# Kernel tuning notes

Hardware: AMD Instinct MI355X
Metric: run time of the kernel (lower is better)

The kernel has to match this reference:

```python
import jax, jax.numpy as jnp
import numpy as np

N = 38332          # poi_len - 1 nodes
POI_LEN = 38333
GF = 64            # graph_features
POI_DIM = 128
C = 128            # gcn_channel
L = 4              # gcn_layers
OUT = 128          # graph_out_dim
E = N * 16         # edges (avg degree 16)
IN_DIM = POI_DIM * GF // 2 + GF // 2  # 4128


def leaky(x, s):
    return jnp.where(x >= 0, x, s * x)


def _gcn(x, W, b, src, dst):
    # PyG GCNConv: lin -> symmetric deg^{-1/2} norm over self-loop graph -> scatter-sum + bias
    h = x @ W
    deg = jax.ops.segment_sum(jnp.ones(src.shape[0], h.dtype), dst, num_segments=N)
    dinv = jnp.where(deg > 0, jax.lax.rsqrt(deg), 0.0)
    norm = dinv[src] * dinv[dst]
    return jax.ops.segment_sum(h[src] * norm[:, None], dst, num_segments=N) + b


def _gat(x, W, a_src, a_dst, b, src, dst):
    # PyG GATConv (heads=1): per-edge LeakyReLU(0.2) logits, softmax over incoming edges
    h = x @ W
    als = h @ a_src            # [N]
    ald = h @ a_dst            # [N]
    e = leaky(als[src] + ald[dst], 0.2)   # [E+N]
    m = jax.ops.segment_max(e, dst, num_segments=N)
    ex = jnp.exp(e - m[dst])
    s = jax.ops.segment_sum(ex, dst, num_segments=N)
    alpha = ex / s[dst]
    return jax.ops.segment_sum(h[src] * alpha[:, None], dst, num_segments=N) + b


def _gnorm(x, w, b, ms, eps=1e-5):
    # PyG GraphNorm over the single graph (node axis)
    mean = x.mean(axis=0)
    out = x - ms * mean
    var = (out * out).mean(axis=0)
    return w * out * jax.lax.rsqrt(var + eps) + b


def setup_inputs() -> dict:
    key = jax.random.key(0)
    ks = jax.random.split(key, 20)
    d = {}
    d["poi"] = jax.random.randint(ks[0], (N, GF // 2), 0, POI_LEN, dtype=jnp.int32)
    d["distance"] = jax.random.uniform(ks[1], (N, GF // 2), dtype=jnp.float32)
    d["edge_index"] = jax.random.randint(ks[2], (2, E), 0, N, dtype=jnp.int32)
    d["emb_table"] = jax.random.normal(ks[3], (POI_LEN, POI_DIM), dtype=jnp.float32) * 0.05
    d["W_in"] = jax.random.normal(ks[4], (IN_DIM, C), dtype=jnp.float32) * 0.02
    d["b_in"] = jnp.zeros((C,), jnp.float32)
    d["gcn_W"] = jax.random.normal(ks[5], (L, C, C), dtype=jnp.float32) * 0.05
    d["gcn_b"] = jnp.zeros((L, C), jnp.float32)
    d["norm_w"] = jnp.ones((L, C), jnp.float32)
    d["norm_b"] = jnp.zeros((L, C), jnp.float32)
    d["norm_ms"] = jnp.ones((L, C), jnp.float32)
    d["gat_W"] = jax.random.normal(ks[6], (L, C, C), dtype=jnp.float32) * 0.05
    d["gat_asrc"] = jax.random.normal(ks[7], (L, C), dtype=jnp.float32) * 0.05
    d["gat_adst"] = jax.random.normal(ks[8], (L, C), dtype=jnp.float32) * 0.05
    d["gat_b"] = jnp.zeros((L, C), jnp.float32)
    d["W_out"] = jax.random.normal(ks[9], (C, 1), dtype=jnp.float32) * 0.05
    d["b_out"] = jnp.zeros((1,), jnp.float32)
    d["fc1_W"] = jax.random.normal(ks[10], (N, 128), dtype=jnp.float32) * 0.01
    d["fc1_b"] = jnp.zeros((128,), jnp.float32)
    d["fc2_W"] = jax.random.normal(ks[11], (128, OUT), dtype=jnp.float32) * 0.05
    d["fc2_b"] = jnp.zeros((OUT,), jnp.float32)
    return d


def reference(poi, distance, edge_index, emb_table, W_in, b_in, gcn_W, gcn_b,
              norm_w, norm_b, norm_ms, gat_W, gat_asrc, gat_adst, gat_b,
              W_out, b_out, fc1_W, fc1_b, fc2_W, fc2_b):
    loops = jnp.arange(N, dtype=edge_index.dtype)
    src = jnp.concatenate([edge_index[0], loops])   # self loops (PyG default)
    dst = jnp.concatenate([edge_index[1], loops])
    # feature assembly: emb(poi) flattened || distance
    x = jnp.concatenate([emb_table[poi].reshape(N, -1), distance], axis=1)  # [N, 4128]
    x = leaky(_gcn(x, W_in, b_in, src, dst), 0.01)
    for i in range(L):  # GcnUnit: GCN->norm->lrelu->res, GAT->norm->lrelu->res (shared norm params)
        t = _gnorm(_gcn(x, gcn_W[i], gcn_b[i], src, dst), norm_w[i], norm_b[i], norm_ms[i])
        x = x + leaky(t, 0.01)
        t = _gnorm(_gat(x, gat_W[i], gat_asrc[i], gat_adst[i], gat_b[i], src, dst),
                   norm_w[i], norm_b[i], norm_ms[i])
        x = x + leaky(t, 0.01)
    x = leaky(_gcn(x, W_out, b_out, src, dst), 0.01).reshape(-1)  # [N]
    h = leaky(x @ fc1_W + fc1_b, 0.01)
    return h @ fc2_W + fc2_b  # [128]
```

## Files before the change

kernel.cpp:

```cpp
#include <hip/hip_runtime.h>


typedef _Float16 f16;
typedef f16 f16x8 __attribute__((ext_vector_type(8)));
typedef f16 f16x4 __attribute__((ext_vector_type(4)));
typedef f16 f16x2 __attribute__((ext_vector_type(2)));
typedef float f32x4 __attribute__((ext_vector_type(4)));

__device__ __forceinline__ float lrelu(float x, float s){ return x>=0.f? x : s*x; }

__global__ __launch_bounds__(256) void k_deg(const int* __restrict__ dst,
                                             int* __restrict__ deg, int E) {
  int i = blockIdx.x * 256 + threadIdx.x;
  if (i < E) atomicAdd(&deg[dst[i]], 1);
}

__global__ __launch_bounds__(1024) void k_scan1(const int* __restrict__ deg,
    int* __restrict__ row_ptr, int* __restrict__ bsum, float* __restrict__ dinv, int n) {
  int b = blockIdx.x, t = threadIdx.x, i = b * 1024 + t;
  __shared__ int sd[1024];
  int v = (i < n) ? deg[i] : 0;
  if (i < n) dinv[i] = rsqrtf((float)(v + 1));
  sd[t] = v;
  __syncthreads();
  for (int off = 1; off < 1024; off <<= 1) {
    int o = (t >= off) ? sd[t - off] : 0;
    __syncthreads();
    sd[t] += o;
    __syncthreads();
  }
  if (i < n) row_ptr[i + 1] = sd[t];
  if (t == 1023) bsum[b] = sd[1023];
  if (b == 0 && t == 0) row_ptr[0] = 0;
}

__global__ __launch_bounds__(64) void k_scan2(int* __restrict__ bsum, int nb) {
  int lane = threadIdx.x;
  int v = (lane < nb) ? bsum[lane] : 0;
  int x = v;
  for (int off = 1; off < 64; off <<= 1) {
    int o = __shfl_up(x, off, 64);
    if (lane >= off) x += o;
  }
  if (lane < nb) bsum[lane] = x - v;
}

__global__ __launch_bounds__(256) void k_scan3(int* __restrict__ row_ptr,
                                               const int* __restrict__ bsum, int n) {
  int i = blockIdx.x * 256 + threadIdx.x;
  if (i < n) row_ptr[i + 1] += bsum[i >> 10];
}

__global__ __launch_bounds__(256) void k_fill(const int* __restrict__ src,
                                              const int* __restrict__ dst,
                                              const int* __restrict__ row_ptr,
                                              const float* __restrict__ dinv,
                                              int* __restrict__ fill,
                                              int* __restrict__ csr,
                                              float* __restrict__ csrw, int E) {
  int i = blockIdx.x * 256 + threadIdx.x;
  if (i < E) {
    int d = dst[i], s = src[i];
    int pos = row_ptr[d] + atomicAdd(&fill[d], 1);
    csr[pos] = s;
    csrw[pos] = dinv[d] * dinv[s];
  }
}

__global__ __launch_bounds__(256) void k_conv_emb(const float* __restrict__ src,
                                                  f16* __restrict__ dst, int total4) {
  int i = blockIdx.x * 256 + threadIdx.x;
  if (i >= total4) return;
  float4 v = ((const float4*)src)[i];
  f16x4 o = { (f16)v.x, (f16)v.y, (f16)v.z, (f16)v.w };
  ((f16x4*)dst)[i] = o;
}

__global__ __launch_bounds__(256) void k_pack_w(const float* __restrict__ W,
    f16* __restrict__ hi, int kb_total) {
  int idx = blockIdx.x * 256 + threadIdx.x;
  int c = idx & 127, kb = idx >> 7;
  if (kb >= kb_total) return;
  f16x8 hv;
#pragma unroll
  for (int j = 0; j < 8; j++) hv[j] = (f16)W[(size_t)(kb*8 + j) * 128 + c];
  ((f16x8*)hi)[idx] = hv;
}

__global__ __launch_bounds__(256) void k_pack_w8(const float* __restrict__ gcnW,
    const float* __restrict__ gatW, f16* __restrict__ hi, f16* __restrict__ lo) {
  int mat = blockIdx.y;
  const float* W = (mat < 4) ? gcnW + (size_t)mat * 16384 : gatW + (size_t)(mat - 4) * 16384;
  int idx = blockIdx.x * 256 + threadIdx.x;
  int c = idx & 127, kb = idx >> 7;
  f16x8 hv, lv;
#pragma unroll
  for (int j = 0; j < 8; j++) {
    float v = W[(size_t)(kb*8 + j) * 128 + c];
    f16 h = (f16)v;
    hv[j] = h; lv[j] = (f16)(v - (float)h);
  }
  ((f16x8*)hi)[mat * 2048 + idx] = hv;
  ((f16x8*)lo)[mat * 2048 + idx] = lv;
}

#define APAD 152
__global__ __launch_bounds__(512) void k_mfma_embed(const int* __restrict__ poi,
    const float* __restrict__ dist, const f16* __restrict__ eh,
    const f16* __restrict__ wh, f16* __restrict__ H16, int n) {
  __shared__ __attribute__((aligned(16))) char smem[49152];
  int* poi_s = (int*)smem;
  f16* aS    = (f16*)(smem + 8192);
  f16* OT    = (f16*)smem;
  float* F   = (float*)(smem + 16384);
  int tid = threadIdx.x;
  int bn = blockIdx.x * 64;
  int half = tid >> 8;
  int t2 = tid & 255;
  int ln = t2 >> 2, qt = t2 & 3;
  int xrow = bn + ln; if (xrow > n - 1) xrow = n - 1;
  {
#pragma unroll
    for (int jj = 0; jj < 4; jj++)
      poi_s[half * 1024 + (qt * 4 + jj) * 64 + ln] =
        poi[(size_t)xrow * 32 + half * 16 + qt * 4 + jj];
  }
  int w2 = (tid >> 6) & 3, lane = tid & 63;
  int q = lane >> 4, l15 = lane & 15;
  int mtb = (w2 & 1) * 2;
  int ntb = (w2 >> 1) * 4;
  f16* aH = aS + half * 64 * APAD;
  f32x4 acc[2][4];
#pragma unroll
  for (int a = 0; a < 2; a++)
#pragma unroll
    for (int b = 0; b < 4; b++) { acc[a][b][0]=0.f; acc[a][b][1]=0.f; acc[a][b][2]=0.f; acc[a][b][3]=0.f; }
  __syncthreads();

  f16x8 r0, r1, r2, r3;
  {
    const f16* srcp = eh + (size_t)poi_s[half * 1024 + ln] * 128 + qt * 32;
    r0 = *(const f16x8*)(srcp);      r1 = *(const f16x8*)(srcp + 8);
    r2 = *(const f16x8*)(srcp + 16); r3 = *(const f16x8*)(srcp + 24);
  }

#pragma unroll 1
  for (int j = 0; j < 16; j++) {
    __syncthreads();
    f16* wp = aH + ln * APAD + qt * 32;
    *(f16x8*)(wp) = r0; *(f16x8*)(wp + 8) = r1;
    *(f16x8*)(wp + 16) = r2; *(f16x8*)(wp + 24) = r3;
    if (j + 1 < 16) {
      const f16* srcp = eh + (size_t)poi_s[half * 1024 + (j + 1) * 64 + ln] * 128 + qt * 32;
      r0 = *(const f16x8*)(srcp);      r1 = *(const f16x8*)(srcp + 8);
      r2 = *(const f16x8*)(srcp + 16); r3 = *(const f16x8*)(srcp + 24);
    }
    __syncthreads();
#pragma unroll
    for (int kcl = 0; kcl < 4; kcl++) {
      f16x8 a_h[2];
#pragma unroll
      for (int mi = 0; mi < 2; mi++)
        a_h[mi] = *(const f16x8*)(aH + ((mtb + mi) * 16 + l15) * APAD + kcl * 32 + q * 8);
      int kb = (half * 16 + j) * 16 + kcl * 4 + q;
#pragma unroll
      for (int ni = 0; ni < 4; ni++) {
        f16x8 bh = *(const f16x8*)(wh + ((size_t)kb * 128 + (ntb + ni) * 16 + l15) * 8);
#pragma unroll
        for (int mi = 0; mi < 2; mi++)
          acc[mi][ni] = __builtin_amdgcn_mfma_f32_16x16x32_f16(a_h[mi], bh, acc[mi][ni], 0, 0, 0);
      }
    }
  }
  if (half) {
    int nc0 = bn + (mtb + 0) * 16 + l15; if (nc0 > n - 1) nc0 = n - 1;
    int nc1 = bn + (mtb + 1) * 16 + l15; if (nc1 > n - 1) nc1 = n - 1;
    f16x8 ad[2];
#pragma unroll
    for (int mi = 0; mi < 2; mi++) {
      int nc = mi ? nc1 : nc0;
      const float* dp = dist + (size_t)nc * 32 + q * 8;
      float4 d0 = *(const float4*)dp, d1 = *(const float4*)(dp + 4);
      ad[mi][0]=(f16)d0.x; ad[mi][1]=(f16)d0.y; ad[mi][2]=(f16)d0.z; ad[mi][3]=(f16)d0.w;
      ad[mi][4]=(f16)d1.x; ad[mi][5]=(f16)d1.y; ad[mi][6]=(f16)d1.z; ad[mi][7]=(f16)d1.w;
    }
    int kb = 512 + q;
#pragma unroll
    for (int ni = 0; ni < 4; ni++) {
      f16x8 bh = *(const f16x8*)(wh + ((size_t)kb * 128 + (ntb + ni) * 16 + l15) * 8);
#pragma unroll
      for (int mi = 0; mi < 2; mi++)
        acc[mi][ni] = __builtin_amdgcn_mfma_f32_16x16x32_f16(ad[mi], bh, acc[mi][ni], 0, 0, 0);
    }
  }
  __syncthreads();
  if (half) {
#pragma unroll
    for (int mi = 0; mi < 2; mi++)
#pragma unroll
      for (int ni = 0; ni < 4; ni++)
#pragma unroll
        for (int r = 0; r < 4; r++)
          F[((mtb + mi) * 16 + q * 4 + r) * 128 + (ntb + ni) * 16 + l15] = acc[mi][ni][r];
  }
  __syncthreads();
  if (!half) {
#pragma unroll
    for (int mi = 0; mi < 2; mi++)
#pragma unroll
      for (int ni = 0; ni < 4; ni++)
#pragma unroll
        for (int r = 0; r < 4; r++) {
          int o = ((mtb + mi) * 16 + q * 4 + r) * 128 + (ntb + ni) * 16 + l15;
          OT[o] = (f16)(acc[mi][ni][r] + F[o]);
        }
  }
  __syncthreads();
#pragma unroll
  for (int ch = 0; ch < 2; ch++) {
    int c1024 = tid + ch * 512;
    int row = c1024 >> 4, c8 = c1024 & 15;
    if (bn + row < n)
      *(f16x8*)(H16 + (size_t)(bn + row) * 128 + c8 * 8) = *(const f16x8*)(OT + row * 128 + c8 * 8);
  }
}

#define LPAD 136
__global__ __launch_bounds__(256) void k_mfma_lin(const f16* __restrict__ XH,
    const f16* __restrict__ wh, const f16* __restrict__ wl,
    f16* __restrict__ H16, int n,
    const float* __restrict__ asrc, const float* __restrict__ adst,
    float* __restrict__ als, float* __restrict__ ald) {
  __shared__ __attribute__((aligned(16))) char smem[64 * LPAD * 2];
  f16* aS = (f16*)smem;
  f16* ot = (f16*)smem;
  float* dsrc = (float*)(smem + 16384);
  float* ddst = (float*)(smem + 16896);
  int tid = threadIdx.x;
  int bn = blockIdx.x * 64;
  int ln = tid >> 2, qt = tid & 3;
  int xrow = bn + ln; if (xrow > n - 1) xrow = n - 1;
  int w = tid >> 6, lane = tid & 63;
  int q = lane >> 4, l15 = lane & 15;
  int mtb = (w & 1) * 2;
  int ntb = (w >> 1) * 4;
  {
    const f16* srcp = XH + (size_t)xrow * 128 + qt * 32;
    f16* wp = aS + ln * LPAD + qt * 32;
    *(f16x8*)(wp)      = *(const f16x8*)(srcp);
    *(f16x8*)(wp + 8)  = *(const f16x8*)(srcp + 8);
    *(f16x8*)(wp + 16) = *(const f16x8*)(srcp + 16);
    *(f16x8*)(wp + 24) = *(const f16x8*)(srcp + 24);
  }
  float av[4], bv[4];
  if (asrc) {
#pragma unroll
    for (int ni = 0; ni < 4; ni++) {
      av[ni] = asrc[(ntb + ni) * 16 + l15];
      bv[ni] = adst[(ntb + ni) * 16 + l15];
    }
  }
  f32x4 acc[2][4];
#pragma unroll
  for (int a = 0; a < 2; a++)
#pragma unroll
    for (int b = 0; b < 4; b++) { acc[a][b][0]=0.f; acc[a][b][1]=0.f; acc[a][b][2]=0.f; acc[a][b][3]=0.f; }
  __syncthreads();
#pragma unroll
  for (int kcl = 0; kcl < 4; kcl++) {
    f16x8 a_h[2];
#pragma unroll
    for (int mi = 0; mi < 2; mi++)
      a_h[mi] = *(const f16x8*)(aS + ((mtb + mi) * 16 + l15) * LPAD + kcl * 32 + q * 8);
    int kb = kcl * 4 + q;
#pragma unroll
    for (int ni = 0; ni < 4; ni++) {
      size_t boff = ((size_t)kb * 128 + (ntb + ni) * 16 + l15) * 8;
      f16x8 bh = *(const f16x8*)(wh + boff);
      f16x8 bl = *(const f16x8*)(wl + boff);
#pragma unroll
      for (int mi = 0; mi < 2; mi++) {
        acc[mi][ni] = __builtin_amdgcn_mfma_f32_16x16x32_f16(a_h[mi], bh, acc[mi][ni], 0, 0, 0);
        acc[mi][ni] = __builtin_amdgcn_mfma_f32_16x16x32_f16(a_h[mi], bl, acc[mi][ni], 0, 0, 0);
      }
    }
  }
  __syncthreads();
  if (asrc) {
#pragma unroll
    for (int mi = 0; mi < 2; mi++)
#pragma unroll
      for (int r = 0; r < 4; r++) {
        float ps = 0.f, pd = 0.f;
#pragma unroll
        for (int ni = 0; ni < 4; ni++) { ps += acc[mi][ni][r] * av[ni]; pd += acc[mi][ni][r] * bv[ni]; }
#pragma unroll
        for (int msk = 8; msk > 0; msk >>= 1) {
          ps += __shfl_xor(ps, msk, 64);
          pd += __shfl_xor(pd, msk, 64);
        }
        if (l15 == 0) {
          int row = (mtb + mi) * 16 + q * 4 + r;
          dsrc[row * 2 + (w >> 1)] = ps;
          ddst[row * 2 + (w >> 1)] = pd;
        }
      }
  }
#pragma unroll
  for (int mi = 0; mi < 2; mi++)
#pragma unroll
    for (int ni = 0; ni < 4; ni++)
#pragma unroll
      for (int r = 0; r < 4; r++)
        ot[((mtb + mi) * 16 + q * 4 + r) * 128 + (ntb + ni) * 16 + l15] = (f16)acc[mi][ni][r];
  __syncthreads();
  if (bn + ln < n) {
    f16* dst = H16 + (size_t)(bn + ln) * 128 + qt * 32;
    const f16* srcp = ot + ln * 128 + qt * 32;
#pragma unroll
    for (int jj = 0; jj < 4; jj++)
      *(f16x8*)(dst + jj * 8) = *(const f16x8*)(srcp + jj * 8);
  }
  if (asrc && tid < 64 && bn + tid < n) {
    als[bn + tid] = dsrc[tid * 2] + dsrc[tid * 2 + 1];
    ald[bn + tid] = ddst[tid * 2] + ddst[tid * 2 + 1];
  }
}

__global__ __launch_bounds__(256) void k_gcn_agg16(const f16x2* __restrict__ H2,
    const float* __restrict__ dinv, const int* __restrict__ row_ptr,
    const int* __restrict__ csr, const float* __restrict__ csrw,
    const float* __restrict__ bias,
    float2* __restrict__ out2, f16x2* __restrict__ xh_out, int n, int leaky_flag,
    float* __restrict__ psum, float* __restrict__ psumsq) {
  int w = threadIdx.x >> 6;
  int node = blockIdx.x * 4 + w;
  int lane = threadIdx.x & 63;
  __shared__ float s1[4][128], s2[4][128];
  float vx = 0.f, vy = 0.f;
  if (node < n) {
    int rs = row_ptr[node], re = row_ptr[node + 1];
    int d = re - rs;
    float dn = dinv[node];
    int  sidx = (lane < d) ? csr[rs + lane]  : 0;
    float swt = (lane < d) ? csrw[rs + lane] : 0.f;
    f16x2 sv = H2[(size_t)node * 64 + lane];
    float ax = dn * dn * (float)sv[0], ay = dn * dn * (float)sv[1];
    int dl = d < 64 ? d : 64;
    int j = 0;
#pragma unroll 4
    for (; j + 3 < dl; j += 4) {
      int i0 = __shfl(sidx, j, 64), i1 = __shfl(sidx, j + 1, 64);
      int i2 = __shfl(sidx, j + 2, 64), i3 = __shfl(sidx, j + 3, 64);
      float w0 = __shfl(swt, j, 64), w1 = __shfl(swt, j + 1, 64);
      float w2 = __shfl(swt, j + 2, 64), w3 = __shfl(swt, j + 3, 64);
      f16x2 v0 = H2[(size_t)i0 * 64 + lane];
      f16x2 v1 = H2[(size_t)i1 * 64 + lane];
      f16x2 v2 = H2[(size_t)i2 * 64 + lane];
      f16x2 v3 = H2[(size_t)i3 * 64 + lane];
      ax += w0*(float)v0[0] + w1*(float)v1[0] + w2*(float)v2[0] + w3*(float)v3[0];
      ay += w0*(float)v0[1] + w1*(float)v1[1] + w2*(float)v2[1] + w3*(float)v3[1];
    }
    for (; j < dl; j++) {
      int ii = __shfl(sidx, j, 64);
      float ww = __shfl(swt, j, 64);
      f16x2 v = H2[(size_t)ii * 64 + lane];
      ax += ww * (float)v[0]; ay += ww * (float)v[1];
    }
    for (int e = rs + 64; e < re; e++) {
      int s = csr[e]; float wv = csrw[e];
      f16x2 v = H2[(size_t)s * 64 + lane];
      ax += wv * (float)v[0]; ay += wv * (float)v[1];
    }
    float2 bvv = ((const float2*)bias)[lane];
    vx = ax + bvv.x; vy = ay + bvv.y;
    if (leaky_flag) { vx = lrelu(vx, 0.01f); vy = lrelu(vy, 0.01f); }
    out2[(size_t)node * 64 + lane] = make_float2(vx, vy);
    if (xh_out) { f16x2 o = { (f16)vx, (f16)vy }; xh_out[(size_t)node * 64 + lane] = o; }
  }
  if (psum) {
    s1[w][2*lane] = vx;  s1[w][2*lane+1] = vy;
    s2[w][2*lane] = vx*vx; s2[w][2*lane+1] = vy*vy;
    __syncthreads();
    int t = threadIdx.x;
    if (t < 128) {
      float S = s1[0][t] + s1[1][t] + s1[2][t] + s1[3][t];
      float Q = s2[0][t] + s2[1][t] + s2[2][t] + s2[3][t];
      int slot = blockIdx.x & 127;
      atomicAdd(&psum[slot * 128 + t], S);
      atomicAdd(&psumsq[slot * 128 + t], Q);
    }
  }
}

__global__ __launch_bounds__(256) void k_gat_agg16(const f16x2* __restrict__ H2,
    const float* __restrict__ als, const float* __restrict__ ald,
    const int* __restrict__ row_ptr, const int* __restrict__ csr,
    const float* __restrict__ bias, float2* __restrict__ y2, int n,
    float* __restrict__ psum, float* __restrict__ psumsq) {
  int w = threadIdx.x >> 6;
  int node = blockIdx.x * 4 + w;
  int lane = threadIdx.x & 63;
  __shared__ float s1[4][128], s2[4][128];
  float vx = 0.f, vy = 0.f;
  if (node < n) {
    int rs = row_ptr[node], re = row_ptr[node + 1];
    int d = re - rs;
    float aldn = ald[node];
    float e_self = lrelu(als[node] + aldn, 0.2f);
    f16x2 sv = H2[(size_t)node * 64 + lane];
    float ax, ay, sm;
    if (d <= 64) {
      int sidx = (lane < d) ? csr[rs + lane] : 0;
      float e_k = (lane < d) ? lrelu(als[sidx] + aldn, 0.2f) : -3.4e38f;
      float tmx = e_k;
      for (int off = 1; off < 64; off <<= 1) tmx = fmaxf(tmx, __shfl_xor(tmx, off, 64));
      float mx = fmaxf(e_self, tmx);
      float g_k = (lane < d) ? __expf(e_k - mx) : 0.f;
      float tsm = g_k;
      for (int off = 1; off < 64; off <<= 1) tsm += __shfl_xor(tsm, off, 64);
      float ws = __expf(e_self - mx);
      sm = tsm + ws;
      ax = ws * (float)sv[0]; ay = ws * (float)sv[1];
      int j = 0;
#pragma unroll 4
      for (; j + 3 < d; j += 4) {
        int i0 = __shfl(sidx, j, 64), i1 = __shfl(sidx, j + 1, 64);
        int i2 = __shfl(sidx, j + 2, 64), i3 = __shfl(sidx, j + 3, 64);
        float g0 = __shfl(g_k, j, 64), g1 = __shfl(g_k, j + 1, 64);
        float g2 = __shfl(g_k, j + 2, 64), g3 = __shfl(g_k, j + 3, 64);
        f16x2 v0 = H2[(size_t)i0 * 64 + lane];
        f16x2 v1 = H2[(size_t)i1 * 64 + lane];
        f16x2 v2 = H2[(size_t)i2 * 64 + lane];
        f16x2 v3 = H2[(size_t)i3 * 64 + lane];
        ax += g0*(float)v0[0] + g1*(float)v1[0] + g2*(float)v2[0] + g3*(float)v3[0];
        ay += g0*(float)v0[1] + g1*(float)v1[1] + g2*(float)v2[1] + g3*(float)v3[1];
      }
      for (; j < d; j++) {
        int ii = __shfl(sidx, j, 64);
        float gg = __shfl(g_k, j, 64);
        f16x2 v = H2[(size_t)ii * 64 + lane];
        ax += gg * (float)v[0]; ay += gg * (float)v[1];
      }
    } else {
      float mx = e_self;
      for (int i = rs + lane; i < re; i += 64) mx = fmaxf(mx, lrelu(als[csr[i]] + aldn, 0.2f));
      for (int off = 1; off < 64; off <<= 1) mx = fmaxf(mx, __shfl_xor(mx, off, 64));
      float ws = __expf(e_self - mx);
      sm = ws;
      ax = ws * (float)sv[0]; ay = ws * (float)sv[1];
      for (int i = rs; i < re; i++) {
        int s = csr[i];
        float g = __expf(lrelu(als[s] + aldn, 0.2f) - mx);
        f16x2 v = H2[(size_t)s * 64 + lane];
        sm += g; ax += g*(float)v[0]; ay += g*(float)v[1];
      }
    }
    float inv_s = 1.f / sm;
    float2 bvv = ((const float2*)bias)[lane];
    vx = ax * inv_s + bvv.x; vy = ay * inv_s + bvv.y;
    y2[(size_t)node * 64 + lane] = make_float2(vx, vy);
  }
  s1[w][2*lane] = vx;  s1[w][2*lane+1] = vy;
  s2[w][2*lane] = vx*vx; s2[w][2*lane+1] = vy*vy;
  __syncthreads();
  int t = threadIdx.x;
  if (t < 128) {
    float S = s1[0][t] + s1[1][t] + s1[2][t] + s1[3][t];
    float Q = s2[0][t] + s2[1][t] + s2[2][t] + s2[3][t];
    int slot = blockIdx.x & 127;
    atomicAdd(&psum[slot * 128 + t], S);
    atomicAdd(&psumsq[slot * 128 + t], Q);
  }
}

__global__ __launch_bounds__(256) void k_stats(const float* __restrict__ psum,
    const float* __restrict__ psumsq, const float* __restrict__ w,
    const float* __restrict__ bb, const float* __restrict__ ms,
    float* __restrict__ scaleA, float* __restrict__ shiftA, int n) {
  int t = threadIdx.x, c = t & 127, half = t >> 7;
  float S = 0.f, Q = 0.f;
  for (int s = half; s < 128; s += 2) { S += psum[s * 128 + c]; Q += psumsq[s * 128 + c]; }
  __shared__ float sh[256], sq[256];
  sh[t] = S; sq[t] = Q;
  __syncthreads();
  if (half == 0) {
    double Sd = (double)sh[c] + (double)sh[c + 128];
    double Qd = (double)sq[c] + (double)sq[c + 128];
    double invn = 1.0 / (double)n;
    double mean = Sd * invn;
    double mt = (double)ms[c] * mean;
    double var = Qd * invn - 2.0 * mt * mean + mt * mt;
    float rstd = rsqrtf((float)var + 1e-5f);
    float sc = w[c] * rstd;
    scaleA[c] = sc;
    shiftA[c] = bb[c] - sc * (float)mt;
  }
}

__global__ __launch_bounds__(256) void k_residual(const float* __restrict__ y,
    const float* __restrict__ scaleA, const float* __restrict__ shiftA,
    float* __restrict__ x, f16x4* __restrict__ xh, int n4) {
  int i = blockIdx.x * 256 + threadIdx.x;
  if (i >= n4) return;
  int c4 = (i & 31) * 4;
  float4 yv = ((const float4*)y)[i];
  float4 xv = ((float4*)x)[i];
  float4 sc = *(const float4*)(scaleA + c4);
  float4 sh = *(const float4*)(shiftA + c4);
  xv.x += lrelu(sc.x * yv.x + sh.x, 0.01f);
  xv.y += lrelu(sc.y * yv.y + sh.y, 0.01f);
  xv.z += lrelu(sc.z * yv.z + sh.z, 0.01f);
  xv.w += lrelu(sc.w * yv.w + sh.w, 0.01f);
  ((float4*)x)[i] = xv;
  if (xh) { f16x4 o = { (f16)xv.x, (f16)xv.y, (f16)xv.z, (f16)xv.w }; xh[i] = o; }
}

__global__ __launch_bounds__(256) void k_dot1(const float* __restrict__ x,
                                              const float* __restrict__ wv,
                                              float* __restrict__ o, int n) {
  int node = blockIdx.x * 4 + (threadIdx.x >> 6);
  int lane = threadIdx.x & 63;
  if (node >= n) return;
  float2 hv = ((const float2*)x)[(size_t)node * 64 + lane];
  float2 v1 = ((const float2*)wv)[lane];
  float s1 = hv.x * v1.x + hv.y * v1.y;
  for (int off = 32; off > 0; off >>= 1) s1 += __shfl_down(s1, off, 64);
  if (lane == 0) o[node] = s1;
}

__global__ __launch_bounds__(256) void k_scalar_agg(const float* __restrict__ xsv,
    const float* __restrict__ dinv, const int* __restrict__ row_ptr,
    const int* __restrict__ csr, const float* __restrict__ csrw,
    const float* __restrict__ b_out, float* __restrict__ xout, int n) {
  int i = blockIdx.x * 256 + threadIdx.x;
  if (i >= n) return;
  float dn = dinv[i];
  float acc = dn * dn * xsv[i];
  int re = row_ptr[i + 1];
  for (int e = row_ptr[i]; e < re; e++)
    acc += csrw[e] * xsv[csr[e]];
  xout[i] = lrelu(acc + b_out[0], 0.01f);
}

__global__ __launch_bounds__(256) void k_fc1(const float* __restrict__ xout,
    const float* __restrict__ fw, float* __restrict__ pfc, int n, int chunk) {
  int b = blockIdx.x, t = threadIdx.x;
  int c = t & 127, half = t >> 7;
  int s0 = b * chunk;
  int s1 = s0 + chunk; if (s1 > n) s1 = n;
  float s = 0.f;
  for (int i = s0 + half; i < s1; i += 2) s += xout[i] * fw[(size_t)i * 128 + c];
  __shared__ float sh[256];
  sh[t] = s; __syncthreads();
  if (half == 0) pfc[b * 128 + c] = sh[c] + sh[c + 128];
}

__global__ __launch_bounds__(128) void k_final(const float* __restrict__ pfc,
    const float* __restrict__ b1, const float* __restrict__ fw2,
    const float* __restrict__ b2, float* __restrict__ out) {
  int c = threadIdx.x;
  float s = 0.f;
  for (int b = 0; b < 128; b++) s += pfc[b * 128 + c];
  float hv = lrelu(s + b1[c], 0.01f);
  __shared__ float h1[128];
  h1[c] = hv; __syncthreads();
  float o = b2[c];
  for (int j = 0; j < 128; j++) o += h1[j] * fw2[j * 128 + c];
  out[c] = o;
}

extern "C" void kernel_launch(void* const* d_in, const int* in_sizes, int n_in,
                              void* d_out, int out_size, void* d_ws, size_t ws_size,
                              hipStream_t stream) {
  const int* poi      = (const int*)d_in[0];
  const float* dist   = (const float*)d_in[1];
  const int* ei       = (const int*)d_in[2];
  const float* emb    = (const float*)d_in[3];
  const float* W_in   = (const float*)d_in[4];
  const float* b_in   = (const float*)d_in[5];
  const float* gcn_W  = (const float*)d_in[6];
  const float* gcn_b  = (const float*)d_in[7];
  const float* norm_w = (const float*)d_in[8];
  const float* norm_b = (const float*)d_in[9];
  const float* norm_ms= (const float*)d_in[10];
  const float* gat_W  = (const float*)d_in[11];
  const float* gat_as = (const float*)d_in[12];
  const float* gat_ad = (const float*)d_in[13];
  const float* gat_b  = (const float*)d_in[14];
  const float* W_out  = (const float*)d_in[15];
  const float* b_out  = (const float*)d_in[16];
  const float* fc1_W  = (const float*)d_in[17];
  const float* fc1_b  = (const float*)d_in[18];
  const float* fc2_W  = (const float*)d_in[19];
  const float* fc2_b  = (const float*)d_in[20];

  const int N   = in_sizes[0] / 32;
  const int E   = in_sizes[2] / 2;
  const int POI = in_sizes[3] / 128;
  const int* srcp = ei;
  const int* dstp = ei + E;
  float* out = (float*)d_out;

  char* p = (char*)d_ws;
  auto alloc = [&](size_t bytes) { char* r = p; p += (bytes + 255) & ~(size_t)255; return r; };
  float* x   = (float*)alloc((size_t)N * 128 * 4);
  f16* h16   = (f16*)alloc((size_t)N * 128 * 2);
  f16* xh    = (f16*)alloc((size_t)N * 128 * 2);
  size_t Rneed = (size_t)POI * 128 * 2;
  size_t Ry    = (size_t)N * 128 * 4;
  char* R = alloc(Rneed > Ry ? Rneed : Ry);
  f16* ehalf = (f16*)R;
  float* y   = (float*)R;
  const int KBIN = 4128 / 8;
  f16* wih = (f16*)alloc((size_t)KBIN * 128 * 8 * 2);
  f16* wsh = (f16*)alloc((size_t)8 * 16384 * 2);
  f16* wsl = (f16*)alloc((size_t)8 * 16384 * 2);
  float* dinv   = (float*)alloc((size_t)N * 4);
  float* als    = (float*)alloc((size_t)N * 4);
  float* ald    = (float*)alloc((size_t)N * 4);
  float* xsv    = (float*)alloc((size_t)N * 4);
  float* xout   = (float*)alloc((size_t)N * 4);
  float* statsbuf = (float*)alloc((size_t)32 * 16384 * 4);
  float* pfc    = (float*)alloc(128 * 128 * 4);
  float* scaleA = (float*)alloc(128 * 4);
  float* shiftA = (float*)alloc(128 * 4);
  int* deg     = (int*)alloc((size_t)N * 2 * 4);
  int* fill    = deg + N;
  int* row_ptr = (int*)alloc(((size_t)N + 1) * 4);
  int* csr     = (int*)alloc((size_t)E * 4);
  float* csrw  = (float*)alloc((size_t)E * 4);
  int* bsum    = (int*)alloc(64 * 4);

  const int chunk = (N + 127) / 128;
  const int gblocks = (N + 63) / 64;
  const int eblocks = (E + 255) / 256;
  const int n4 = N * 32;
  const int nwb = (N + 3) / 4;
  const int nb1024 = (N + 1023) / 1024;

  hipMemsetAsync(deg, 0, sizeof(int) * 2 * (size_t)N, stream);
  hipMemsetAsync(statsbuf, 0, (size_t)32 * 16384 * 4, stream);
  k_deg<<<eblocks, 256, 0, stream>>>(dstp, deg, E);
  k_scan1<<<nb1024, 1024, 0, stream>>>(deg, row_ptr, bsum, dinv, N);
  k_scan2<<<1, 64, 0, stream>>>(bsum, nb1024);
  k_scan3<<<(N + 255) / 256, 256, 0, stream>>>(row_ptr, bsum, N);
  k_fill<<<eblocks, 256, 0, stream>>>(srcp, dstp, row_ptr, dinv, fill, csr, csrw, E);

  int et4 = POI * 128 / 4;
  k_conv_emb<<<(et4 + 255) / 256, 256, 0, stream>>>(emb, ehalf, et4);
  k_pack_w<<<(KBIN * 128 + 255) / 256, 256, 0, stream>>>(W_in, wih, KBIN);
  k_pack_w8<<<dim3(8, 8), 256, 0, stream>>>(gcn_W, gat_W, wsh, wsl);

  k_mfma_embed<<<gblocks, 512, 0, stream>>>(poi, dist, ehalf, wih, h16, N);
  k_gcn_agg16<<<nwb, 256, 0, stream>>>((const f16x2*)h16, dinv, row_ptr, csr, csrw, b_in,
                                       (float2*)x, (f16x2*)xh, N, 1, nullptr, nullptr);

  for (int l = 0; l < 4; l++) {
    const f16* gh = wsh + (size_t)l * 16384;
    const f16* gl = wsl + (size_t)l * 16384;
    const f16* th = wsh + (size_t)(4 + l) * 16384;
    const f16* tl = wsl + (size_t)(4 + l) * 16384;
    float* ps0 = statsbuf + (size_t)(4 * l) * 16384;
    float* pq0 = ps0 + 16384;
    float* ps1 = ps0 + 2 * 16384;
    float* pq1 = ps0 + 3 * 16384;
    k_mfma_lin<<<gblocks, 256, 0, stream>>>(xh, gh, gl, h16, N,
                                            (const float*)nullptr, (const float*)nullptr,
                                            (float*)nullptr, (float*)nullptr);
    k_gcn_agg16<<<nwb, 256, 0, stream>>>((const f16x2*)h16, dinv, row_ptr, csr, csrw,
                                         gcn_b + l * 128, (float2*)y, (f16x2*)nullptr, N, 0,
                                         ps0, pq0);
    k_stats<<<1, 256, 0, stream>>>(ps0, pq0, norm_w + l * 128, norm_b + l * 128,
                                   norm_ms + l * 128, scaleA, shiftA, N);
    k_residual<<<(n4 + 255) / 256, 256, 0, stream>>>(y, scaleA, shiftA, x, (f16x4*)xh, n4);
    k_mfma_lin<<<gblocks, 256, 0, stream>>>(xh, th, tl, h16, N,
                                            gat_as + l * 128, gat_ad + l * 128, als, ald);
    k_gat_agg16<<<nwb, 256, 0, stream>>>((const f16x2*)h16, als, ald, row_ptr, csr,
                                         gat_b + l * 128, (float2*)y, N, ps1, pq1);
    k_stats<<<1, 256, 0, stream>>>(ps1, pq1, norm_w + l * 128, norm_b + l * 128,
                                   norm_ms + l * 128, scaleA, shiftA, N);
    k_residual<<<(n4 + 255) / 256, 256, 0, stream>>>(y, scaleA, shiftA, x,
        (l == 3) ? (f16x4*)nullptr : (f16x4*)xh, n4);
  }

  k_dot1<<<nwb, 256, 0, stream>>>(x, W_out, xsv, N);
  k_scalar_agg<<<(N + 255) / 256, 256, 0, stream>>>(xsv, dinv, row_ptr, csr, csrw, b_out, xout, N);
  k_fc1<<<128, 256, 0, stream>>>(xout, fc1_W, pfc, N, chunk);
  k_final<<<1, 128, 0, stream>>>(pfc, fc1_b, fc2_W, fc2_b, out);
}
```

Measured before the change: 1.023 ms.

## Split node features into column halves and fuse residual into linear kernel

Node feature matrices are now stored as two column-half planes of 64 f16 each. The aggregation kernels launch twice as many blocks, each handling one half, which shrinks the gathered row to 128 bytes and may improve cache hit rates on random neighbor gathers. The standalone residual kernel is removed: the norm-scale, leaky ReLU and residual update are fused into the staging step of the next linear (MFMA) kernel, and into the final dot kernel, which saves a full pass over the activations. In exchange each half-pass re-reads the CSR indices and weights and does more atomics for the statistics.

```diff
diff --git a/kernel.cpp b/kernel.cpp
--- a/kernel.cpp
+++ b/kernel.cpp
@@ -220,8 +220,10 @@
   for (int ch = 0; ch < 2; ch++) {
     int c1024 = tid + ch * 512;
     int row = c1024 >> 4, c8 = c1024 & 15;
-    if (bn + row < n)
-      *(f16x8*)(H16 + (size_t)(bn + row) * 128 + c8 * 8) = *(const f16x8*)(OT + row * 128 + c8 * 8);
+    if (bn + row < n) {
+      f16* dstp = H16 + (size_t)(c8 >> 3) * ((size_t)n * 64) + (size_t)(bn + row) * 64 + (c8 & 7) * 8;
+      *(f16x8*)dstp = *(const f16x8*)(OT + row * 128 + c8 * 8);
+    }
   }
 }
 
@@ -230,7 +232,9 @@
     const f16* __restrict__ wh, const f16* __restrict__ wl,
     f16* __restrict__ H16, int n,
     const float* __restrict__ asrc, const float* __restrict__ adst,
-    float* __restrict__ als, float* __restrict__ ald) {
+    float* __restrict__ als, float* __restrict__ ald,
+    const float* __restrict__ yres, const float* __restrict__ scA,
+    const float* __restrict__ shA, float* __restrict__ xf) {
   __shared__ __attribute__((aligned(16))) char smem[64 * LPAD * 2];
   f16* aS = (f16*)smem;
   f16* ot = (f16*)smem;
@@ -239,14 +243,37 @@
   int tid = threadIdx.x;
   int bn = blockIdx.x * 64;
   int ln = tid >> 2, qt = tid & 3;
-  int xrow = bn + ln; if (xrow > n - 1) xrow = n - 1;
   int w = tid >> 6, lane = tid & 63;
   int q = lane >> 4, l15 = lane & 15;
   int mtb = (w & 1) * 2;
   int ntb = (w >> 1) * 4;
-  {
+  f16* wp = aS + ln * LPAD + qt * 32;
+  if (yres) {
+    int row = bn + ln;
+    if (row < n) {
+      const float4* yp = (const float4*)(yres + (size_t)row * 128 + qt * 32);
+      float4* xp = (float4*)(xf + (size_t)row * 128 + qt * 32);
+      const float4* scp = (const float4*)(scA + qt * 32);
+      const float4* shp = (const float4*)(shA + qt * 32);
+#pragma unroll
+      for (int jj = 0; jj < 8; jj++) {
+        float4 yv = yp[jj], xv = xp[jj], sc = scp[jj], sh = shp[jj];
+        xv.x += lrelu(sc.x * yv.x + sh.x, 0.01f);
+        xv.y += lrelu(sc.y * yv.y + sh.y, 0.01f);
+        xv.z += lrelu(sc.z * yv.z + sh.z, 0.01f);
+        xv.w += lrelu(sc.w * yv.w + sh.w, 0.01f);
+        xp[jj] = xv;
+        f16x4 o = { (f16)xv.x, (f16)xv.y, (f16)xv.z, (f16)xv.w };
+        *(f16x4*)(wp + jj * 4) = o;
+      }
+    } else {
+      f16x8 z = {};
+#pragma unroll
+      for (int jj = 0; jj < 4; jj++) *(f16x8*)(wp + jj * 8) = z;
+    }
+  } else {
+    int xrow = bn + ln; if (xrow > n - 1) xrow = n - 1;
     const f16* srcp = XH + (size_t)xrow * 128 + qt * 32;
-    f16* wp = aS + ln * LPAD + qt * 32;
     *(f16x8*)(wp)      = *(const f16x8*)(srcp);
     *(f16x8*)(wp + 8)  = *(const f16x8*)(srcp + 8);
     *(f16x8*)(wp + 16) = *(const f16x8*)(srcp + 16);
@@ -315,11 +342,11 @@
         ot[((mtb + mi) * 16 + q * 4 + r) * 128 + (ntb + ni) * 16 + l15] = (f16)acc[mi][ni][r];
   __syncthreads();
   if (bn + ln < n) {
-    f16* dst = H16 + (size_t)(bn + ln) * 128 + qt * 32;
     const f16* srcp = ot + ln * 128 + qt * 32;
+    f16* dstp = H16 + (size_t)(qt >> 1) * ((size_t)n * 64) + (size_t)(bn + ln) * 64 + (qt & 1) * 32;
 #pragma unroll
     for (int jj = 0; jj < 4; jj++)
-      *(f16x8*)(dst + jj * 8) = *(const f16x8*)(srcp + jj * 8);
+      *(f16x8*)(dstp + jj * 8) = *(const f16x8*)(srcp + jj * 8);
   }
   if (asrc && tid < 64 && bn + tid < n) {
     als[bn + tid] = dsrc[tid * 2] + dsrc[tid * 2 + 1];
@@ -327,25 +354,27 @@
   }
 }
 
-__global__ __launch_bounds__(256) void k_gcn_agg16(const f16x2* __restrict__ H2,
+__global__ __launch_bounds__(256) void k_gcn_agg16(const f16* __restrict__ H,
     const float* __restrict__ dinv, const int* __restrict__ row_ptr,
     const int* __restrict__ csr, const float* __restrict__ csrw,
     const float* __restrict__ bias,
-    float2* __restrict__ out2, f16x2* __restrict__ xh_out, int n, int leaky_flag,
-    float* __restrict__ psum, float* __restrict__ psumsq) {
+    float* __restrict__ yout, f16* __restrict__ xh_out, int n, int nwb,
+    int leaky_flag, float* __restrict__ psum, float* __restrict__ psumsq) {
   int w = threadIdx.x >> 6;
-  int node = blockIdx.x * 4 + w;
+  int bx = blockIdx.x;
+  int pass = (bx >= nwb) ? 1 : 0;
+  int node = (bx - pass * nwb) * 4 + w;
   int lane = threadIdx.x & 63;
-  __shared__ float s1[4][128], s2[4][128];
-  float vx = 0.f, vy = 0.f;
+  const f16* Hh = H + (size_t)pass * ((size_t)n * 64);
+  __shared__ float s1[4][64], s2[4][64];
+  float vx = 0.f;
   if (node < n) {
     int rs = row_ptr[node], re = row_ptr[node + 1];
     int d = re - rs;
     float dn = dinv[node];
     int  sidx = (lane < d) ? csr[rs + lane]  : 0;
     float swt = (lane < d) ? csrw[rs + lane] : 0.f;
-    f16x2 sv = H2[(size_t)node * 64 + lane];
-    float ax = dn * dn * (float)sv[0], ay = dn * dn * (float)sv[1];
+    float ax = dn * dn * (float)Hh[(size_t)node * 64 + lane];
     int dl = d < 64 ? d : 64;
     int j = 0;
 #pragma unroll 4
@@ -354,62 +383,59 @@
       int i2 = __shfl(sidx, j + 2, 64), i3 = __shfl(sidx, j + 3, 64);
       float w0 = __shfl(swt, j, 64), w1 = __shfl(swt, j + 1, 64);
       float w2 = __shfl(swt, j + 2, 64), w3 = __shfl(swt, j + 3, 64);
-      f16x2 v0 = H2[(size_t)i0 * 64 + lane];
-      f16x2 v1 = H2[(size_t)i1 * 64 + lane];
-      f16x2 v2 = H2[(size_t)i2 * 64 + lane];
-      f16x2 v3 = H2[(size_t)i3 * 64 + lane];
-      ax += w0*(float)v0[0] + w1*(float)v1[0] + w2*(float)v2[0] + w3*(float)v3[0];
-      ay += w0*(float)v0[1] + w1*(float)v1[1] + w2*(float)v2[1] + w3*(float)v3[1];
+      float v0 = (float)Hh[(size_t)i0 * 64 + lane];
+      float v1 = (float)Hh[(size_t)i1 * 64 + lane];
+      float v2 = (float)Hh[(size_t)i2 * 64 + lane];
+      float v3 = (float)Hh[(size_t)i3 * 64 + lane];
+      ax += w0*v0 + w1*v1 + w2*v2 + w3*v3;
     }
     for (; j < dl; j++) {
       int ii = __shfl(sidx, j, 64);
       float ww = __shfl(swt, j, 64);
-      f16x2 v = H2[(size_t)ii * 64 + lane];
-      ax += ww * (float)v[0]; ay += ww * (float)v[1];
+      ax += ww * (float)Hh[(size_t)ii * 64 + lane];
     }
     for (int e = rs + 64; e < re; e++) {
-      int s = csr[e]; float wv = csrw[e];
-      f16x2 v = H2[(size_t)s * 64 + lane];
-      ax += wv * (float)v[0]; ay += wv * (float)v[1];
-    }
-    float2 bvv = ((const float2*)bias)[lane];
-    vx = ax + bvv.x; vy = ay + bvv.y;
-    if (leaky_flag) { vx = lrelu(vx, 0.01f); vy = lrelu(vy, 0.01f); }
-    out2[(size_t)node * 64 + lane] = make_float2(vx, vy);
-    if (xh_out) { f16x2 o = { (f16)vx, (f16)vy }; xh_out[(size_t)node * 64 + lane] = o; }
+      ax += csrw[e] * (float)Hh[(size_t)csr[e] * 64 + lane];
+    }
+    vx = ax + bias[pass * 64 + lane];
+    if (leaky_flag) vx = lrelu(vx, 0.01f);
+    yout[(size_t)node * 128 + pass * 64 + lane] = vx;
+    if (xh_out) xh_out[(size_t)node * 128 + pass * 64 + lane] = (f16)vx;
   }
   if (psum) {
-    s1[w][2*lane] = vx;  s1[w][2*lane+1] = vy;
-    s2[w][2*lane] = vx*vx; s2[w][2*lane+1] = vy*vy;
+    s1[w][lane] = vx; s2[w][lane] = vx * vx;
     __syncthreads();
     int t = threadIdx.x;
-    if (t < 128) {
+    if (t < 64) {
       float S = s1[0][t] + s1[1][t] + s1[2][t] + s1[3][t];
       float Q = s2[0][t] + s2[1][t] + s2[2][t] + s2[3][t];
-      int slot = blockIdx.x & 127;
-      atomicAdd(&psum[slot * 128 + t], S);
-      atomicAdd(&psumsq[slot * 128 + t], Q);
-    }
-  }
-}
-
-__global__ __launch_bounds__(256) void k_gat_agg16(const f16x2* __restrict__ H2,
+      int slot = bx & 127;
+      atomicAdd(&psum[slot * 128 + pass * 64 + t], S);
+      atomicAdd(&psumsq[slot * 128 + pass * 64 + t], Q);
+    }
+  }
+}
+
+__global__ __launch_bounds__(256) void k_gat_agg16(const f16* __restrict__ H,
     const float* __restrict__ als, const float* __restrict__ ald,
     const int* __restrict__ row_ptr, const int* __restrict__ csr,
-    const float* __restrict__ bias, float2* __restrict__ y2, int n,
+    const float* __restrict__ bias, float* __restrict__ yout, int n, int nwb,
     float* __restrict__ psum, float* __restrict__ psumsq) {
   int w = threadIdx.x >> 6;
-  int node = blockIdx.x * 4 + w;
+  int bx = blockIdx.x;
+  int pass = (bx >= nwb) ? 1 : 0;
+  int node = (bx - pass * nwb) * 4 + w;
   int lane = threadIdx.x & 63;
-  __shared__ float s1[4][128], s2[4][128];
-  float vx = 0.f, vy = 0.f;
+  const f16* Hh = H + (size_t)pass * ((size_t)n * 64);
+  __shared__ float s1[4][64], s2[4][64];
+  float vx = 0.f;
   if (node < n) {
     int rs = row_ptr[node], re = row_ptr[node + 1];
     int d = re - rs;
     float aldn = ald[node];
     float e_self = lrelu(als[node] + aldn, 0.2f);
-    f16x2 sv = H2[(size_t)node * 64 + lane];
-    float ax, ay, sm;
+    float sv = (float)Hh[(size_t)node * 64 + lane];
+    float ax, sm;
     if (d <= 64) {
       int sidx = (lane < d) ? csr[rs + lane] : 0;
       float e_k = (lane < d) ? lrelu(als[sidx] + aldn, 0.2f) : -3.4e38f;
@@ -421,7 +447,7 @@
       for (int off = 1; off < 64; off <<= 1) tsm += __shfl_xor(tsm, off, 64);
       float ws = __expf(e_self - mx);
       sm = tsm + ws;
-      ax = ws * (float)sv[0]; ay = ws * (float)sv[1];
+      ax = ws * sv;
       int j = 0;
 #pragma unroll 4
       for (; j + 3 < d; j += 4) {
@@ -429,18 +455,16 @@
         int i2 = __shfl(sidx, j + 2, 64), i3 = __shfl(sidx, j + 3, 64);
         float g0 = __shfl(g_k, j, 64), g1 = __shfl(g_k, j + 1, 64);
         float g2 = __shfl(g_k, j + 2, 64), g3 = __shfl(g_k, j + 3, 64);
-        f16x2 v0 = H2[(size_t)i0 * 64 + lane];
-        f16x2 v1 = H2[(size_t)i1 * 64 + lane];
-        f16x2 v2 = H2[(size_t)i2 * 64 + lane];
-        f16x2 v3 = H2[(size_t)i3 * 64 + lane];
-        ax += g0*(float)v0[0] + g1*(float)v1[0] + g2*(float)v2[0] + g3*(float)v3[0];
-        ay += g0*(float)v0[1] + g1*(float)v1[1] + g2*(float)v2[1] + g3*(float)v3[1];
+        float v0 = (float)Hh[(size_t)i0 * 64 + lane];
+        float v1 = (float)Hh[(size_t)i1 * 64 + lane];
+        float v2 = (float)Hh[(size_t)i2 * 64 + lane];
+        float v3 = (float)Hh[(size_t)i3 * 64 + lane];
+        ax += g0*v0 + g1*v1 + g2*v2 + g3*v3;
       }
       for (; j < d; j++) {
         int ii = __shfl(sidx, j, 64);
         float gg = __shfl(g_k, j, 64);
-        f16x2 v = H2[(size_t)ii * 64 + lane];
-        ax += gg * (float)v[0]; ay += gg * (float)v[1];
+        ax += gg * (float)Hh[(size_t)ii * 64 + lane];
       }
     } else {
       float mx = e_self;
@@ -448,29 +472,26 @@
       for (int off = 1; off < 64; off <<= 1) mx = fmaxf(mx, __shfl_xor(mx, off, 64));
       float ws = __expf(e_self - mx);
       sm = ws;
-      ax = ws * (float)sv[0]; ay = ws * (float)sv[1];
+      ax = ws * sv;
       for (int i = rs; i < re; i++) {
         int s = csr[i];
         float g = __expf(lrelu(als[s] + aldn, 0.2f) - mx);
-        f16x2 v = H2[(size_t)s * 64 + lane];
-        sm += g; ax += g*(float)v[0]; ay += g*(float)v[1];
+        sm += g; ax += g * (float)Hh[(size_t)s * 64 + lane];
       }
     }
     float inv_s = 1.f / sm;
-    float2 bvv = ((const float2*)bias)[lane];
-    vx = ax * inv_s + bvv.x; vy = ay * inv_s + bvv.y;
-    y2[(size_t)node * 64 + lane] = make_float2(vx, vy);
-  }
-  s1[w][2*lane] = vx;  s1[w][2*lane+1] = vy;
-  s2[w][2*lane] = vx*vx; s2[w][2*lane+1] = vy*vy;
+    vx = ax * inv_s + bias[pass * 64 + lane];
+    yout[(size_t)node * 128 + pass * 64 + lane] = vx;
+  }
+  s1[w][lane] = vx; s2[w][lane] = vx * vx;
   __syncthreads();
   int t = threadIdx.x;
-  if (t < 128) {
+  if (t < 64) {
     float S = s1[0][t] + s1[1][t] + s1[2][t] + s1[3][t];
     float Q = s2[0][t] + s2[1][t] + s2[2][t] + s2[3][t];
-    int slot = blockIdx.x & 127;
-    atomicAdd(&psum[slot * 128 + t], S);
-    atomicAdd(&psumsq[slot * 128 + t], Q);
+    int slot = bx & 127;
+    atomicAdd(&psum[slot * 128 + pass * 64 + t], S);
+    atomicAdd(&psumsq[slot * 128 + pass * 64 + t], Q);
   }
 }
 
@@ -498,33 +519,21 @@
   }
 }
 
-__global__ __launch_bounds__(256) void k_residual(const float* __restrict__ y,
-    const float* __restrict__ scaleA, const float* __restrict__ shiftA,
-    float* __restrict__ x, f16x4* __restrict__ xh, int n4) {
-  int i = blockIdx.x * 256 + threadIdx.x;
-  if (i >= n4) return;
-  int c4 = (i & 31) * 4;
-  float4 yv = ((const float4*)y)[i];
-  float4 xv = ((float4*)x)[i];
-  float4 sc = *(const float4*)(scaleA + c4);
-  float4 sh = *(const float4*)(shiftA + c4);
-  xv.x += lrelu(sc.x * yv.x + sh.x, 0.01f);
-  xv.y += lrelu(sc.y * yv.y + sh.y, 0.01f);
-  xv.z += lrelu(sc.z * yv.z + sh.z, 0.01f);
-  xv.w += lrelu(sc.w * yv.w + sh.w, 0.01f);
-  ((float4*)x)[i] = xv;
-  if (xh) { f16x4 o = { (f16)xv.x, (f16)xv.y, (f16)xv.z, (f16)xv.w }; xh[i] = o; }
-}
-
-__global__ __launch_bounds__(256) void k_dot1(const float* __restrict__ x,
-                                              const float* __restrict__ wv,
-                                              float* __restrict__ o, int n) {
+__global__ __launch_bounds__(256) void k_dot1_res(const float* __restrict__ y,
+    const float* __restrict__ scA, const float* __restrict__ shA,
+    const float* __restrict__ x, const float* __restrict__ wv,
+    float* __restrict__ o, int n) {
   int node = blockIdx.x * 4 + (threadIdx.x >> 6);
   int lane = threadIdx.x & 63;
   if (node >= n) return;
-  float2 hv = ((const float2*)x)[(size_t)node * 64 + lane];
+  float2 yv = ((const float2*)y)[(size_t)node * 64 + lane];
+  float2 xv = ((const float2*)x)[(size_t)node * 64 + lane];
+  float2 sc = ((const float2*)scA)[lane];
+  float2 sh = ((const float2*)shA)[lane];
+  float hx = xv.x + lrelu(sc.x * yv.x + sh.x, 0.01f);
+  float hy = xv.y + lrelu(sc.y * yv.y + sh.y, 0.01f);
   float2 v1 = ((const float2*)wv)[lane];
-  float s1 = hv.x * v1.x + hv.y * v1.y;
+  float s1 = hx * v1.x + hy * v1.y;
   for (int off = 32; off > 0; off >>= 1) s1 += __shfl_down(s1, off, 64);
   if (lane == 0) o[node] = s1;
 }
@@ -635,7 +644,6 @@
   const int chunk = (N + 127) / 128;
   const int gblocks = (N + 63) / 64;
   const int eblocks = (E + 255) / 256;
-  const int n4 = N * 32;
   const int nwb = (N + 3) / 4;
   const int nb1024 = (N + 1023) / 1024;
 
@@ -653,8 +661,8 @@
   k_pack_w8<<<dim3(8, 8), 256, 0, stream>>>(gcn_W, gat_W, wsh, wsl);
 
   k_mfma_embed<<<gblocks, 512, 0, stream>>>(poi, dist, ehalf, wih, h16, N);
-  k_gcn_agg16<<<nwb, 256, 0, stream>>>((const f16x2*)h16, dinv, row_ptr, csr, csrw, b_in,
-                                       (float2*)x, (f16x2*)xh, N, 1, nullptr, nullptr);
+  k_gcn_agg16<<<2 * nwb, 256, 0, stream>>>(h16, dinv, row_ptr, csr, csrw, b_in,
+                                           x, xh, N, nwb, 1, nullptr, nullptr);
 
   for (int l = 0; l < 4; l++) {
     const f16* gh = wsh + (size_t)l * 16384;
@@ -665,26 +673,26 @@
     float* pq0 = ps0 + 16384;
     float* ps1 = ps0 + 2 * 16384;
     float* pq1 = ps0 + 3 * 16384;
-    k_mfma_lin<<<gblocks, 256, 0, stream>>>(xh, gh, gl, h16, N,
-                                            (const float*)nullptr, (const float*)nullptr,
-                                            (float*)nullptr, (float*)nullptr);
-    k_gcn_agg16<<<nwb, 256, 0, stream>>>((const f16x2*)h16, dinv, row_ptr, csr, csrw,
-                                         gcn_b + l * 128, (float2*)y, (f16x2*)nullptr, N, 0,
-                                         ps0, pq0);
+    if (l == 0)
+      k_mfma_lin<<<gblocks, 256, 0, stream>>>(xh, gh, gl, h16, N,
+          nullptr, nullptr, nullptr, nullptr, nullptr, nullptr, nullptr, nullptr);
+    else
+      k_mfma_lin<<<gblocks, 256, 0, stream>>>(nullptr, gh, gl, h16, N,
+          nullptr, nullptr, nullptr, nullptr, y, scaleA, shiftA, x);
+    k_gcn_agg16<<<2 * nwb, 256, 0, stream>>>(h16, dinv, row_ptr, csr, csrw,
+                                             gcn_b + l * 128, y, (f16*)nullptr, N, nwb, 0,
+                                             ps0, pq0);
     k_stats<<<1, 256, 0, stream>>>(ps0, pq0, norm_w + l * 128, norm_b + l * 128,
                                    norm_ms + l * 128, scaleA, shiftA, N);
-    k_residual<<<(n4 + 255) / 256, 256, 0, stream>>>(y, scaleA, shiftA, x, (f16x4*)xh, n4);
-    k_mfma_lin<<<gblocks, 256, 0, stream>>>(xh, th, tl, h16, N,
-                                            gat_as + l * 128, gat_ad + l * 128, als, ald);
-    k_gat_agg16<<<nwb, 256, 0, stream>>>((const f16x2*)h16, als, ald, row_ptr, csr,
-                                         gat_b + l * 128, (float2*)y, N, ps1, pq1);
+    k_mfma_lin<<<gblocks, 256, 0, stream>>>(nullptr, th, tl, h16, N,
+        gat_as + l * 128, gat_ad + l * 128, als, ald, y, scaleA, shiftA, x);
+    k_gat_agg16<<<2 * nwb, 256, 0, stream>>>(h16, als, ald, row_ptr, csr,
+                                             gat_b + l * 128, y, N, nwb, ps1, pq1);
     k_stats<<<1, 256, 0, stream>>>(ps1, pq1, norm_w + l * 128, norm_b + l * 128,
                                    norm_ms + l * 128, scaleA, shiftA, N);
-    k_residual<<<(n4 + 255) / 256, 256, 0, stream>>>(y, scaleA, shiftA, x,
-        (l == 3) ? (f16x4*)nullptr : (f16x4*)xh, n4);
-  }
-
-  k_dot1<<<nwb, 256, 0, stream>>>(x, W_out, xsv, N);
+  }
+
+  k_dot1_res<<<nwb, 256, 0, stream>>>(y, scaleA, shiftA, x, W_out, xsv, N);
   k_scalar_agg<<<(N + 255) / 256, 256, 0, stream>>>(xsv, dinv, row_ptr, csr, csrw, b_out, xout, N);
   k_fc1<<<128, 256, 0, stream>>>(xout, fc1_W, pfc, N, chunk);
   k_final<<<1, 128, 0, stream>>>(pfc, fc1_b, fc2_W, fc2_b, out);
```

Measured after the change: 1.185 ms. +15.8%, slower.
